# Kernel optimization log

Hardware: AMD Instinct MI355X
Metric: run time of the kernel (lower is better)

Reference implementation:

```python
import jax, jax.numpy as jnp
import numpy as np

D = 768      # hidden_size
H = 12       # num_attention_heads
HD = D // H  # head_dim
B, S = 1, 4096


def setup_inputs() -> dict:
    key = jax.random.key(0)
    ks = jax.random.split(key, 9)
    s_in = 1.0 / np.sqrt(D)
    s_o = 1.0 / np.sqrt(D)
    x = jax.random.normal(ks[0], (B, S, D), dtype=jnp.float32)
    # per-head Q/K/V projections stacked: [H, D, HD]
    Wq = jax.random.uniform(ks[1], (H, D, HD), jnp.float32, -s_in, s_in)
    Wk = jax.random.uniform(ks[2], (H, D, HD), jnp.float32, -s_in, s_in)
    Wv = jax.random.uniform(ks[3], (H, D, HD), jnp.float32, -s_in, s_in)
    bq = jax.random.uniform(ks[4], (H, HD), jnp.float32, -s_in, s_in)
    bk = jax.random.uniform(ks[5], (H, HD), jnp.float32, -s_in, s_in)
    bv = jax.random.uniform(ks[6], (H, HD), jnp.float32, -s_in, s_in)
    Wo = jax.random.uniform(ks[7], (D, D), jnp.float32, -s_o, s_o)
    bo = jax.random.uniform(ks[8], (D,), jnp.float32, -s_o, s_o)
    return {"hidden_states": x, "Wq": Wq, "Wk": Wk, "Wv": Wv,
            "bq": bq, "bk": bk, "bv": bv, "Wo": Wo, "bo": bo}


def reference(hidden_states, Wq, Wk, Wv, bq, bk, bv, Wo, bo):
    x = hidden_states  # [B, S, D]
    # fused per-head projections -> [B, H, S, HD]
    q = jnp.einsum('bsd,hde->bhse', x, Wq) + bq[None, :, None, :]
    k = jnp.einsum('bsd,hde->bhse', x, Wk) + bk[None, :, None, :]
    v = jnp.einsum('bsd,hde->bhse', x, Wv) + bv[None, :, None, :]
    scale = 1.0 / jnp.sqrt(jnp.asarray(HD, q.dtype))
    scores = jnp.einsum('bhse,bhte->bhst', q, k) * scale  # [B, H, S, S]
    weights = jax.nn.softmax(scores, axis=-1)
    attn = jnp.einsum('bhst,bhte->bhse', weights, v)  # [B, H, S, HD]
    # concat heads along feature dim -> [B, S, D]
    concat = attn.transpose(0, 2, 1, 3).reshape(x.shape[0], x.shape[1], H * HD)
    return concat @ Wo + bo
```

## Files before the change

### kernel.cpp

```cpp
#include <hip/hip_runtime.h>

#define SLEN 4096
#define DMODEL 768
#define NH 12
#define HD 64
#define NQKV 2304
#define KDIM 768
#define KVBLK 64
#define NT (SLEN / KVBLK)

typedef _Float16 f16x8 __attribute__((ext_vector_type(8)));
typedef _Float16 f16x4v __attribute__((ext_vector_type(4)));
typedef float f32x4 __attribute__((ext_vector_type(4)));
typedef float f32x16 __attribute__((ext_vector_type(16)));

__device__ __forceinline__ void async16(void* lds, const void* g) {
  __builtin_amdgcn_global_load_lds((const __attribute__((address_space(1))) void*)g,
                                   (__attribute__((address_space(3))) void*)lds, 16, 0, 0);
}

__device__ __forceinline__ void plswap(unsigned& a, unsigned& b) {
  auto r = __builtin_amdgcn_permlane32_swap(a, b, false, false);
  a = r[0];
  b = r[1];
}

__device__ __forceinline__ unsigned pk(float a, float b) {
  auto r = __builtin_amdgcn_cvt_pkrtz(a, b);
  return __builtin_bit_cast(unsigned, r);
}

__global__ __launch_bounds__(256) void pack_kernel(
    const float* __restrict__ x, const float* __restrict__ Wq, const float* __restrict__ Wk,
    const float* __restrict__ Wv, const float* __restrict__ Wo,
    _Float16* __restrict__ xb, _Float16* __restrict__ wqkvt, _Float16* __restrict__ wot) {
  int tid = blockIdx.x * 256 + threadIdx.x;
  int stride = gridDim.x * 256;
  int n4 = SLEN * DMODEL / 4;
  for (int i = tid; i < n4; i += stride) {
    float4 v = ((const float4*)x)[i];
    f16x4v o = {(_Float16)v.x, (_Float16)v.y, (_Float16)v.z, (_Float16)v.w};
    ((f16x4v*)xb)[i] = o;
  }
  n4 = NQKV * DMODEL / 4;
  for (int i = tid; i < n4; i += stride) {
    int col = i / (DMODEL / 4);
    int d = (i - col * (DMODEL / 4)) * 4;
    int which = col / DMODEL;
    int cc = col - which * DMODEL;
    int h = cc >> 6, e = cc & 63;
    const float* W = which == 0 ? Wq : (which == 1 ? Wk : Wv);
    const float* s = W + (h * DMODEL + d) * HD + e;
    f16x4v o = {(_Float16)s[0], (_Float16)s[HD], (_Float16)s[2 * HD], (_Float16)s[3 * HD]};
    ((f16x4v*)wqkvt)[i] = o;
  }
  n4 = DMODEL * DMODEL / 4;
  for (int i = tid; i < n4; i += stride) {
    int o_ = i / (DMODEL / 4);
    int d = (i - o_ * (DMODEL / 4)) * 4;
    const float* s = Wo + d * DMODEL + o_;
    f16x4v o = {(_Float16)s[0], (_Float16)s[DMODEL], (_Float16)s[2 * DMODEL], (_Float16)s[3 * DMODEL]};
    ((f16x4v*)wot)[i] = o;
  }
}

__device__ __forceinline__ void gemm_core(const _Float16* __restrict__ A,
                                          const _Float16* __restrict__ Bt,
                                          _Float16* As, _Float16* Bs,
                                          f32x4 (&acc)[4][4], int m0, int n0) {
  int t = threadIdx.x;
  int lane = t & 63, w = t >> 6;
  int lr = lane & 15, lg = lane >> 4;
  int wr = w >> 1, wc = w & 1;
  for (int kb = 0; kb < KDIM / 64; ++kb) {
    #pragma unroll
    for (int i = 0; i < 4; ++i) {
      int base = (w * 4 + i) * 512;
      int off = base + lane * 8;
      int row = off >> 6, col = off & 63;
      async16(&As[base], A + (m0 + row) * KDIM + kb * 64 + col);
      async16(&Bs[base], Bt + (n0 + row) * KDIM + kb * 64 + col);
    }
    __syncthreads();
    #pragma unroll
    for (int kk = 0; kk < 2; ++kk) {
      f16x8 af[4], bf[4];
      #pragma unroll
      for (int mi = 0; mi < 4; ++mi)
        af[mi] = *(const f16x8*)&As[(wr * 64 + mi * 16 + lr) * 64 + kk * 32 + lg * 8];
      #pragma unroll
      for (int ni = 0; ni < 4; ++ni)
        bf[ni] = *(const f16x8*)&Bs[(wc * 64 + ni * 16 + lr) * 64 + kk * 32 + lg * 8];
      #pragma unroll
      for (int mi = 0; mi < 4; ++mi)
        #pragma unroll
        for (int ni = 0; ni < 4; ++ni)
          acc[mi][ni] = __builtin_amdgcn_mfma_f32_16x16x32_f16(af[mi], bf[ni], acc[mi][ni], 0, 0, 0);
    }
    __syncthreads();
  }
}

__global__ __launch_bounds__(256) void gemm_qkv(
    const _Float16* __restrict__ xb, const _Float16* __restrict__ wqkvt,
    const float* __restrict__ bq, const float* __restrict__ bk, const float* __restrict__ bv,
    _Float16* __restrict__ qd, _Float16* __restrict__ kd, _Float16* __restrict__ vtd) {
  __shared__ __align__(16) _Float16 As[128 * 64];
  __shared__ __align__(16) _Float16 Bs[128 * 64];
  f32x4 acc[4][4] = {};
  int m0 = blockIdx.y * 128, n0 = blockIdx.x * 128;
  gemm_core(xb, wqkvt, As, Bs, acc, m0, n0);
  int t = threadIdx.x, lane = t & 63, w = t >> 6;
  int lr = lane & 15, lg = lane >> 4;
  int wr = w >> 1, wc = w & 1;
  int which = n0 / DMODEL;
  const float* bias = which == 0 ? bq : (which == 1 ? bk : bv);
  #pragma unroll
  for (int mi = 0; mi < 4; ++mi)
    #pragma unroll
    for (int ni = 0; ni < 4; ++ni)
      #pragma unroll
      for (int r = 0; r < 4; ++r) {
        int srow = m0 + wr * 64 + mi * 16 + lg * 4 + r;
        int col = n0 + wc * 64 + ni * 16 + lr;
        int cc = col - which * DMODEL;
        int h = cc >> 6, e = cc & 63;
        float val = acc[mi][ni][r] + bias[cc];
        if (which < 2) {
          (which ? kd : qd)[h * (SLEN * HD) + srow * HD + e] = (_Float16)val;
        } else {
          vtd[h * (SLEN * HD) + e * SLEN + srow] = (_Float16)val;
        }
      }
}

__global__ __launch_bounds__(128) void attn_kernel(
    const _Float16* __restrict__ qd, const _Float16* __restrict__ kd,
    const _Float16* __restrict__ vtd, _Float16* __restrict__ attn) {
  __shared__ __align__(16) _Float16 Ks[2][KVBLK * HD];
  __shared__ __align__(16) _Float16 Vts[2][HD * KVBLK];
  int wg = blockIdx.x;
  int orig = (wg & 7) * 96 + (wg >> 3);
  int qb = orig & 63, h = orig >> 6;
  int t = threadIdx.x, lane = t & 63, w = t >> 6;
  int ql = lane & 31, hi = lane >> 5;

  const _Float16* kbase = kd + h * (SLEN * HD);
  const _Float16* vbase = vtd + h * (SLEN * HD);

  auto stage = [&](int bi, int jb) {
    #pragma unroll
    for (int i = 0; i < 4; ++i) {
      int c = (w * 4 + i) * 64 + lane;
      int row = c >> 3;
      int sb = ((c & 7) * 16) ^ ((row & 7) << 4);
      async16(&Ks[bi][(w * 4 + i) * 512], kbase + (jb * KVBLK + row) * HD + sb / 2);
      async16(&Vts[bi][(w * 4 + i) * 512], vbase + row * SLEN + jb * KVBLK + sb / 2);
    }
  };

  int qrow = qb * 64 + w * 32 + ql;
  const _Float16* qp = qd + h * (SLEN * HD) + qrow * HD;
  f16x8 qf[4];
  #pragma unroll
  for (int dblk = 0; dblk < 4; ++dblk)
    qf[dblk] = *(const f16x8*)(qp + dblk * 16 + hi * 8);

  f32x16 oacc[2] = {};
  float mrow = -1e30f, lrow = 0.f;
  const float C = 0.18033688f;
  const float THR = 44.4f;

  stage(0, 0);
  __syncthreads();
  int buf = 0;
  for (int jb = 0; jb < NT; ++jb) {
    if (jb + 1 < NT) stage(buf ^ 1, jb + 1);

    f32x16 sacc[2] = {};
    __builtin_amdgcn_s_setprio(1);
    #pragma unroll
    for (int kblk = 0; kblk < 2; ++kblk)
      #pragma unroll
      for (int dblk = 0; dblk < 4; ++dblk) {
        int off = ((kblk * 32 + ql) * 128 + dblk * 32 + hi * 16) ^ ((ql & 7) << 4);
        f16x8 kf = *(const f16x8*)((const char*)Ks[buf] + off);
        sacc[kblk] = __builtin_amdgcn_mfma_f32_32x32x16_f16(kf, qf[dblk], sacc[kblk], 0, 0, 0);
      }
    __builtin_amdgcn_s_setprio(0);

    float mb = sacc[0][0];
    #pragma unroll
    for (int r = 1; r < 16; ++r) mb = fmaxf(mb, sacc[0][r]);
    #pragma unroll
    for (int r = 0; r < 16; ++r) mb = fmaxf(mb, sacc[1][r]);
    {
      unsigned a = __builtin_bit_cast(unsigned, mb), b = a;
      plswap(a, b);
      mb = fmaxf(__builtin_bit_cast(float, a), __builtin_bit_cast(float, b));
    }
    if (!__all(mb <= mrow + THR)) {
      float mn = fmaxf(mrow, mb);
      float corr = __builtin_amdgcn_exp2f((mrow - mn) * C);
      lrow *= corr;
      #pragma unroll
      for (int r = 0; r < 16; ++r) { oacc[0][r] *= corr; oacc[1][r] *= corr; }
      mrow = mn;
    }
    float negm = -mrow * C;
    float p0[16], p1[16], ps = 0.f;
    #pragma unroll
    for (int r = 0; r < 16; ++r) { p0[r] = __builtin_amdgcn_exp2f(fmaf(sacc[0][r], C, negm)); ps += p0[r]; }
    #pragma unroll
    for (int r = 0; r < 16; ++r) { p1[r] = __builtin_amdgcn_exp2f(fmaf(sacc[1][r], C, negm)); ps += p1[r]; }
    lrow += ps;

    f16x8 pb[4];
    #pragma unroll
    for (int kblk = 0; kblk < 2; ++kblk) {
      const float* pp = kblk ? p1 : p0;
      #pragma unroll
      for (int u = 0; u < 2; ++u) {
        unsigned a0 = pk(pp[8 * u + 0], pp[8 * u + 1]);
        unsigned b0 = pk(pp[8 * u + 4], pp[8 * u + 5]);
        unsigned a1 = pk(pp[8 * u + 2], pp[8 * u + 3]);
        unsigned b1 = pk(pp[8 * u + 6], pp[8 * u + 7]);
        plswap(a0, b0);
        plswap(a1, b1);
        union { unsigned wd[4]; f16x8 v; } uu;
        uu.wd[0] = a0; uu.wd[1] = a1; uu.wd[2] = b0; uu.wd[3] = b1;
        pb[kblk * 2 + u] = uu.v;
      }
    }

    __builtin_amdgcn_s_setprio(1);
    #pragma unroll
    for (int kb16 = 0; kb16 < 4; ++kb16)
      #pragma unroll
      for (int eblk = 0; eblk < 2; ++eblk) {
        int off = ((eblk * 32 + ql) * 128 + kb16 * 32 + hi * 16) ^ ((ql & 7) << 4);
        f16x8 vf = *(const f16x8*)((const char*)Vts[buf] + off);
        oacc[eblk] = __builtin_amdgcn_mfma_f32_32x32x16_f16(vf, pb[kb16], oacc[eblk], 0, 0, 0);
      }
    __builtin_amdgcn_s_setprio(0);
    __syncthreads();
    buf ^= 1;
  }

  {
    unsigned a = __builtin_bit_cast(unsigned, lrow), b = a;
    plswap(a, b);
    lrow = __builtin_bit_cast(float, a) + __builtin_bit_cast(float, b);
  }
  float inv = 1.f / lrow;
  _Float16* ob = attn + qrow * DMODEL + h * HD;
  #pragma unroll
  for (int eblk = 0; eblk < 2; ++eblk)
    #pragma unroll
    for (int i = 0; i < 4; ++i) {
      unsigned w0 = pk(oacc[eblk][4 * i + 0] * inv, oacc[eblk][4 * i + 1] * inv);
      unsigned w1 = pk(oacc[eblk][4 * i + 2] * inv, oacc[eblk][4 * i + 3] * inv);
      union { unsigned wd[2]; f16x4v v; } uu;
      uu.wd[0] = w0; uu.wd[1] = w1;
      *(f16x4v*)(ob + eblk * 32 + 8 * i + 4 * hi) = uu.v;
    }
}

__global__ __launch_bounds__(256) void gemm_out(
    const _Float16* __restrict__ attn, const _Float16* __restrict__ wot,
    const float* __restrict__ bo, float* __restrict__ out) {
  __shared__ __align__(16) _Float16 As[128 * 64];
  __shared__ __align__(16) _Float16 Bs[128 * 64];
  f32x4 acc[4][4] = {};
  int m0 = blockIdx.y * 128, n0 = blockIdx.x * 128;
  gemm_core(attn, wot, As, Bs, acc, m0, n0);
  int t = threadIdx.x, lane = t & 63, w = t >> 6;
  int lr = lane & 15, lg = lane >> 4;
  int wr = w >> 1, wc = w & 1;
  #pragma unroll
  for (int mi = 0; mi < 4; ++mi)
    #pragma unroll
    for (int ni = 0; ni < 4; ++ni)
      #pragma unroll
      for (int r = 0; r < 4; ++r) {
        int srow = m0 + wr * 64 + mi * 16 + lg * 4 + r;
        int col = n0 + wc * 64 + ni * 16 + lr;
        out[srow * DMODEL + col] = acc[mi][ni][r] + bo[col];
      }
}

extern "C" void kernel_launch(void* const* d_in, const int* in_sizes, int n_in,
                              void* d_out, int out_size, void* d_ws, size_t ws_size,
                              hipStream_t stream) {
  const float* x  = (const float*)d_in[0];
  const float* Wq = (const float*)d_in[1];
  const float* Wk = (const float*)d_in[2];
  const float* Wv = (const float*)d_in[3];
  const float* bq = (const float*)d_in[4];
  const float* bk = (const float*)d_in[5];
  const float* bv = (const float*)d_in[6];
  const float* Wo = (const float*)d_in[7];
  const float* bo = (const float*)d_in[8];
  float* out = (float*)d_out;

  char* ws = (char*)d_ws;
  size_t off = 0;
  auto alloc = [&](size_t bytes) {
    char* p = ws + off;
    off += (bytes + 255) & ~size_t(255);
    return p;
  };
  _Float16* xb    = (_Float16*)alloc((size_t)SLEN * DMODEL * 2);
  _Float16* wqkvt = (_Float16*)alloc((size_t)NQKV * DMODEL * 2);
  _Float16* wot   = (_Float16*)alloc((size_t)DMODEL * DMODEL * 2);
  _Float16* qd    = (_Float16*)alloc((size_t)NH * SLEN * HD * 2);
  _Float16* kd    = (_Float16*)alloc((size_t)NH * SLEN * HD * 2);
  _Float16* vtd   = (_Float16*)alloc((size_t)NH * SLEN * HD * 2);
  _Float16* attn  = (_Float16*)alloc((size_t)SLEN * DMODEL * 2);

  hipLaunchKernelGGL(pack_kernel, dim3(1024), dim3(256), 0, stream,
                     x, Wq, Wk, Wv, Wo, xb, wqkvt, wot);
  hipLaunchKernelGGL(gemm_qkv, dim3(NQKV / 128, SLEN / 128), dim3(256), 0, stream,
                     xb, wqkvt, bq, bk, bv, qd, kd, vtd);
  hipLaunchKernelGGL(attn_kernel, dim3(768), dim3(128), 0, stream,
                     qd, kd, vtd, attn);
  hipLaunchKernelGGL(gemm_out, dim3(DMODEL / 128, SLEN / 128), dim3(256), 0, stream,
                     attn, wot, bo, out);
}
```

Measured before the change: 270.0 us.

## Split KV block across two wave pairs in attention with LDS merge

Doubles the attention workgroup to 256 threads. Each pair of waves now processes half of each 64-key tile, cutting per-wave MFMA and softmax work per iteration and adding waves per CU to hide latency. At the end the two partial softmax states (max, sum, output) are merged through shared memory. This adds LDS usage, an extra barrier and a merge epilogue, and the per-key-half max tracking can trigger rescaling more often.

```diff
diff --git a/kernel.cpp b/kernel.cpp
--- a/kernel.cpp
+++ b/kernel.cpp
@@ -134,15 +134,18 @@
       }
 }
 
-__global__ __launch_bounds__(128) void attn_kernel(
+__global__ __launch_bounds__(256, 3) void attn_kernel(
     const _Float16* __restrict__ qd, const _Float16* __restrict__ kd,
     const _Float16* __restrict__ vtd, _Float16* __restrict__ attn) {
   __shared__ __align__(16) _Float16 Ks[2][KVBLK * HD];
   __shared__ __align__(16) _Float16 Vts[2][HD * KVBLK];
+  __shared__ float Om[2][64][32];
+  __shared__ float Mm[2][32], Lm[2][32];
   int wg = blockIdx.x;
   int orig = (wg & 7) * 96 + (wg >> 3);
   int qb = orig & 63, h = orig >> 6;
   int t = threadIdx.x, lane = t & 63, w = t >> 6;
+  int wq = w & 1, wk = w >> 1;
   int ql = lane & 31, hi = lane >> 5;
 
   const _Float16* kbase = kd + h * (SLEN * HD);
@@ -150,16 +153,16 @@
 
   auto stage = [&](int bi, int jb) {
     #pragma unroll
-    for (int i = 0; i < 4; ++i) {
-      int c = (w * 4 + i) * 64 + lane;
+    for (int i = 0; i < 2; ++i) {
+      int c = (w * 2 + i) * 64 + lane;
       int row = c >> 3;
       int sb = ((c & 7) * 16) ^ ((row & 7) << 4);
-      async16(&Ks[bi][(w * 4 + i) * 512], kbase + (jb * KVBLK + row) * HD + sb / 2);
-      async16(&Vts[bi][(w * 4 + i) * 512], vbase + row * SLEN + jb * KVBLK + sb / 2);
+      async16(&Ks[bi][(w * 2 + i) * 512], kbase + (jb * KVBLK + row) * HD + sb / 2);
+      async16(&Vts[bi][(w * 2 + i) * 512], vbase + row * SLEN + jb * KVBLK + sb / 2);
     }
   };
 
-  int qrow = qb * 64 + w * 32 + ql;
+  int qrow = qb * 64 + wq * 32 + ql;
   const _Float16* qp = qd + h * (SLEN * HD) + qrow * HD;
   f16x8 qf[4];
   #pragma unroll
@@ -177,23 +180,19 @@
   for (int jb = 0; jb < NT; ++jb) {
     if (jb + 1 < NT) stage(buf ^ 1, jb + 1);
 
-    f32x16 sacc[2] = {};
+    f32x16 sacc = {};
     __builtin_amdgcn_s_setprio(1);
     #pragma unroll
-    for (int kblk = 0; kblk < 2; ++kblk)
-      #pragma unroll
-      for (int dblk = 0; dblk < 4; ++dblk) {
-        int off = ((kblk * 32 + ql) * 128 + dblk * 32 + hi * 16) ^ ((ql & 7) << 4);
-        f16x8 kf = *(const f16x8*)((const char*)Ks[buf] + off);
-        sacc[kblk] = __builtin_amdgcn_mfma_f32_32x32x16_f16(kf, qf[dblk], sacc[kblk], 0, 0, 0);
-      }
+    for (int dblk = 0; dblk < 4; ++dblk) {
+      int off = ((wk * 32 + ql) * 128 + dblk * 32 + hi * 16) ^ ((ql & 7) << 4);
+      f16x8 kf = *(const f16x8*)((const char*)Ks[buf] + off);
+      sacc = __builtin_amdgcn_mfma_f32_32x32x16_f16(kf, qf[dblk], sacc, 0, 0, 0);
+    }
     __builtin_amdgcn_s_setprio(0);
 
-    float mb = sacc[0][0];
-    #pragma unroll
-    for (int r = 1; r < 16; ++r) mb = fmaxf(mb, sacc[0][r]);
-    #pragma unroll
-    for (int r = 0; r < 16; ++r) mb = fmaxf(mb, sacc[1][r]);
+    float mb = sacc[0];
+    #pragma unroll
+    for (int r = 1; r < 16; ++r) mb = fmaxf(mb, sacc[r]);
     {
       unsigned a = __builtin_bit_cast(unsigned, mb), b = a;
       plswap(a, b);
@@ -208,39 +207,33 @@
       mrow = mn;
     }
     float negm = -mrow * C;
-    float p0[16], p1[16], ps = 0.f;
-    #pragma unroll
-    for (int r = 0; r < 16; ++r) { p0[r] = __builtin_amdgcn_exp2f(fmaf(sacc[0][r], C, negm)); ps += p0[r]; }
-    #pragma unroll
-    for (int r = 0; r < 16; ++r) { p1[r] = __builtin_amdgcn_exp2f(fmaf(sacc[1][r], C, negm)); ps += p1[r]; }
+    float p[16], ps = 0.f;
+    #pragma unroll
+    for (int r = 0; r < 16; ++r) { p[r] = __builtin_amdgcn_exp2f(fmaf(sacc[r], C, negm)); ps += p[r]; }
     lrow += ps;
 
-    f16x8 pb[4];
-    #pragma unroll
-    for (int kblk = 0; kblk < 2; ++kblk) {
-      const float* pp = kblk ? p1 : p0;
-      #pragma unroll
-      for (int u = 0; u < 2; ++u) {
-        unsigned a0 = pk(pp[8 * u + 0], pp[8 * u + 1]);
-        unsigned b0 = pk(pp[8 * u + 4], pp[8 * u + 5]);
-        unsigned a1 = pk(pp[8 * u + 2], pp[8 * u + 3]);
-        unsigned b1 = pk(pp[8 * u + 6], pp[8 * u + 7]);
-        plswap(a0, b0);
-        plswap(a1, b1);
-        union { unsigned wd[4]; f16x8 v; } uu;
-        uu.wd[0] = a0; uu.wd[1] = a1; uu.wd[2] = b0; uu.wd[3] = b1;
-        pb[kblk * 2 + u] = uu.v;
-      }
+    f16x8 pb[2];
+    #pragma unroll
+    for (int u = 0; u < 2; ++u) {
+      unsigned a0 = pk(p[8 * u + 0], p[8 * u + 1]);
+      unsigned b0 = pk(p[8 * u + 4], p[8 * u + 5]);
+      unsigned a1 = pk(p[8 * u + 2], p[8 * u + 3]);
+      unsigned b1 = pk(p[8 * u + 6], p[8 * u + 7]);
+      plswap(a0, b0);
+      plswap(a1, b1);
+      union { unsigned wd[4]; f16x8 v; } uu;
+      uu.wd[0] = a0; uu.wd[1] = a1; uu.wd[2] = b0; uu.wd[3] = b1;
+      pb[u] = uu.v;
     }
 
     __builtin_amdgcn_s_setprio(1);
     #pragma unroll
-    for (int kb16 = 0; kb16 < 4; ++kb16)
+    for (int u = 0; u < 2; ++u)
       #pragma unroll
       for (int eblk = 0; eblk < 2; ++eblk) {
-        int off = ((eblk * 32 + ql) * 128 + kb16 * 32 + hi * 16) ^ ((ql & 7) << 4);
+        int off = ((eblk * 32 + ql) * 128 + wk * 64 + u * 32 + hi * 16) ^ ((ql & 7) << 4);
         f16x8 vf = *(const f16x8*)((const char*)Vts[buf] + off);
-        oacc[eblk] = __builtin_amdgcn_mfma_f32_32x32x16_f16(vf, pb[kb16], oacc[eblk], 0, 0, 0);
+        oacc[eblk] = __builtin_amdgcn_mfma_f32_32x32x16_f16(vf, pb[u], oacc[eblk], 0, 0, 0);
       }
     __builtin_amdgcn_s_setprio(0);
     __syncthreads();
@@ -252,18 +245,44 @@
     plswap(a, b);
     lrow = __builtin_bit_cast(float, a) + __builtin_bit_cast(float, b);
   }
-  float inv = 1.f / lrow;
-  _Float16* ob = attn + qrow * DMODEL + h * HD;
-  #pragma unroll
-  for (int eblk = 0; eblk < 2; ++eblk)
-    #pragma unroll
-    for (int i = 0; i < 4; ++i) {
-      unsigned w0 = pk(oacc[eblk][4 * i + 0] * inv, oacc[eblk][4 * i + 1] * inv);
-      unsigned w1 = pk(oacc[eblk][4 * i + 2] * inv, oacc[eblk][4 * i + 3] * inv);
-      union { unsigned wd[2]; f16x4v v; } uu;
-      uu.wd[0] = w0; uu.wd[1] = w1;
-      *(f16x4v*)(ob + eblk * 32 + 8 * i + 4 * hi) = uu.v;
-    }
+
+  if (wk == 1) {
+    Mm[wq][ql] = mrow;
+    Lm[wq][ql] = lrow;
+    #pragma unroll
+    for (int eblk = 0; eblk < 2; ++eblk)
+      #pragma unroll
+      for (int r = 0; r < 16; ++r) {
+        int e = eblk * 32 + (r & 3) + 8 * (r >> 2) + 4 * hi;
+        Om[wq][e][ql] = oacc[eblk][r];
+      }
+  }
+  __syncthreads();
+  if (wk == 0) {
+    float m1 = Mm[wq][ql], l1 = Lm[wq][ql];
+    float m = fmaxf(mrow, m1);
+    float c0 = __builtin_amdgcn_exp2f((mrow - m) * C);
+    float c1 = __builtin_amdgcn_exp2f((m1 - m) * C);
+    float inv = 1.f / (lrow * c0 + l1 * c1);
+    _Float16* ob = attn + qrow * DMODEL + h * HD;
+    #pragma unroll
+    for (int eblk = 0; eblk < 2; ++eblk) {
+      float om[16];
+      #pragma unroll
+      for (int r = 0; r < 16; ++r) {
+        int e = eblk * 32 + (r & 3) + 8 * (r >> 2) + 4 * hi;
+        om[r] = (oacc[eblk][r] * c0 + Om[wq][e][ql] * c1) * inv;
+      }
+      #pragma unroll
+      for (int i = 0; i < 4; ++i) {
+        unsigned w0 = pk(om[4 * i + 0], om[4 * i + 1]);
+        unsigned w1 = pk(om[4 * i + 2], om[4 * i + 3]);
+        union { unsigned wd[2]; f16x4v v; } uu;
+        uu.wd[0] = w0; uu.wd[1] = w1;
+        *(f16x4v*)(ob + eblk * 32 + 8 * i + 4 * hi) = uu.v;
+      }
+    }
+  }
 }
 
 __global__ __launch_bounds__(256) void gemm_out(
@@ -322,7 +341,7 @@
                      x, Wq, Wk, Wv, Wo, xb, wqkvt, wot);
   hipLaunchKernelGGL(gemm_qkv, dim3(NQKV / 128, SLEN / 128), dim3(256), 0, stream,
                      xb, wqkvt, bq, bk, bv, qd, kd, vtd);
-  hipLaunchKernelGGL(attn_kernel, dim3(768), dim3(128), 0, stream,
+  hipLaunchKernelGGL(attn_kernel, dim3(768), dim3(256), 0, stream,
                      qd, kd, vtd, attn);
   hipLaunchKernelGGL(gemm_out, dim3(DMODEL / 128, SLEN / 128), dim3(256), 0, stream,
                      attn, wot, bo, out);
```

New measurement: 242.1 us. 10.3% less time.
